# Kernel optimization log

Measured on AMD Instinct MI355X. Metric: run time of the kernel, lower is better.

## Reference

```python
import jax, jax.numpy as jnp
import numpy as np

B, N, G, M = 16, 2048, 128, 32
DM, NL, DI, DS, DTR, DC = 384, 12, 768, 16, 24, 4
EPS = 1e-5


def _silu(x):
    return x * jax.nn.sigmoid(x)


def _ln(x, w, b):
    mu = x.mean(-1, keepdims=True)
    v = ((x - mu) ** 2).mean(-1, keepdims=True)
    return (x - mu) * jax.lax.rsqrt(v + EPS) * w + b


def _bn_eval(x, g, b):
    # eval-mode BatchNorm1d (running mean=0, var=1)
    return x * (g * jax.lax.rsqrt(jnp.float32(1.0) + EPS)) + b


def _fps(pts):
    # farthest point sampling, pts [N,3] -> [G] indices (starts at index 0)
    n = pts.shape[0]
    def body(carry, _):
        dmin, i = carry
        dd = jnp.sum((pts - pts[i]) ** 2, -1)
        dmin = jnp.minimum(dmin, dd)
        return (dmin, jnp.argmax(dmin).astype(jnp.int32)), i
    init = (jnp.full((n,), 1e10, pts.dtype), jnp.array(0, jnp.int32))
    (_, _), idx = jax.lax.scan(body, init, None, length=G)
    return idx


def _group(xyz):
    cidx = jax.vmap(_fps)(xyz)                                   # [B,G]
    center = jnp.take_along_axis(xyz, cidx[..., None], axis=1)    # [B,G,3]
    d2 = jnp.sum((center[:, :, None, :] - xyz[:, None, :, :]) ** 2, -1)  # [B,G,N]
    _, nidx = jax.lax.top_k(-d2, M)                               # [B,G,M]
    nb = jax.vmap(lambda p, i: p[i])(xyz, nidx)                   # [B,G,M,3]
    return nb - center[:, :, None, :], center


def _mixer(x, in_w, cw, cb, xp_w, dt_w, dt_b, A_log, Dp, out_w):
    b, L, _ = x.shape
    xz = jnp.einsum('bld,ed->ble', x, in_w)                       # [B,L,2*DI]
    xin, z = xz[..., :DI], xz[..., DI:]
    xpad = jnp.pad(xin, ((0, 0), (DC - 1, 0), (0, 0)))            # causal depthwise conv
    xin = _silu(sum(xpad[:, k:k + L, :] * cw[:, k] for k in range(DC)) + cb)
    dbl = jnp.einsum('bld,ed->ble', xin, xp_w)                    # [B,L,DTR+2*DS]
    dt = jax.nn.softplus(jnp.einsum('blr,dr->bld', dbl[..., :DTR], dt_w) + dt_b)
    Bm, Cm = dbl[..., DTR:DTR + DS], dbl[..., DTR + DS:]
    A = -jnp.exp(A_log)                                           # [DI,DS]
    dA = jnp.exp(dt[..., None] * A)                               # [B,L,DI,DS]
    dBx = (dt * xin)[..., None] * Bm[:, :, None, :]               # [B,L,DI,DS]
    def step(h, inp):
        dA_t, dBx_t, C_t = inp
        h = dA_t * h + dBx_t
        return h, jnp.einsum('bds,bs->bd', h, C_t)
    h0 = jnp.zeros((b, DI, DS), x.dtype)
    _, ys = jax.lax.scan(step, h0, (jnp.swapaxes(dA, 0, 1), jnp.swapaxes(dBx, 0, 1), jnp.swapaxes(Cm, 0, 1)))
    y = jnp.swapaxes(ys, 0, 1) + Dp * xin
    return jnp.einsum('bld,ed->ble', y * _silu(z), out_w)


def forward_fn(xyz, e1w1, e1b1, bn1g, bn1b, e1w2, e1b2, e2w1, e2b1, bn2g, bn2b,
               e2w2, e2b2, pw1, pb1, pw2, pb2, in_w, conv_w, conv_b, xp_w,
               dt_w, dt_b, A_log, Dp, out_w, lnw, lnb, fnw, fnb):
    nb, center = _group(xyz)
    # Encoder (1x1 convs == pointwise linears) over [B*G, M, 3]
    x = nb.reshape(B * G, M, 3)
    f = jax.nn.relu(_bn_eval(x @ e1w1.T + e1b1, bn1g, bn1b))
    f = f @ e1w2.T + e1b2                                         # [BG,M,256]
    fg = f.max(axis=1, keepdims=True)
    f = jnp.concatenate([jnp.broadcast_to(fg, (B * G, M, 256)), f], -1)
    f = jax.nn.relu(_bn_eval(f @ e2w1.T + e2b1, bn2g, bn2b))
    f = f @ e2w2.T + e2b2                                         # [BG,M,DM]
    tokens = f.max(axis=1).reshape(B, G, DM)
    pos = jax.nn.gelu(center @ pw1.T + pb1) @ pw2.T + pb2
    h = tokens + pos
    residual = None
    for i in range(NL):
        residual = h + residual if residual is not None else h
        h = _mixer(_ln(residual, lnw[i], lnb[i]), in_w[i], conv_w[i], conv_b[i],
                   xp_w[i], dt_w[i], dt_b[i], A_log[i], Dp[i], out_w[i])
    return _ln(h + residual, fnw, fnb)


def setup_inputs() -> dict:
    ks = jax.random.split(jax.random.key(0), 16)
    r = lambda i, s, sc=0.02: jax.random.normal(ks[i], s, jnp.float32) * sc
    dt_init = float(np.log(np.expm1(0.01)))
    return {
        'xyz': jax.random.normal(ks[0], (B, N, 3), jnp.float32),
        'e1w1': r(1, (128, 3), 0.3), 'e1b1': jnp.zeros(128),
        'bn1g': jnp.ones(128), 'bn1b': jnp.zeros(128),
        'e1w2': r(2, (256, 128), 0.05), 'e1b2': jnp.zeros(256),
        'e2w1': r(3, (512, 512), 0.03), 'e2b1': jnp.zeros(512),
        'bn2g': jnp.ones(512), 'bn2b': jnp.zeros(512),
        'e2w2': r(4, (DM, 512), 0.03), 'e2b2': jnp.zeros(DM),
        'pw1': r(5, (128, 3), 0.3), 'pb1': jnp.zeros(128),
        'pw2': r(6, (DM, 128), 0.05), 'pb2': jnp.zeros(DM),
        'in_w': r(7, (NL, 2 * DI, DM)),
        'conv_w': r(8, (NL, DI, DC), 0.2), 'conv_b': jnp.zeros((NL, DI)),
        'xp_w': r(9, (NL, DTR + 2 * DS, DI)),
        'dt_w': r(10, (NL, DI, DTR), 0.1),
        'dt_b': jnp.full((NL, DI), dt_init, jnp.float32),
        'A_log': jnp.log(jnp.broadcast_to(jnp.arange(1, DS + 1, dtype=jnp.float32), (NL, DI, DS)) + 0.0),
        'Dp': jnp.ones((NL, DI)),
        'out_w': r(11, (NL, DM, DI)),
        'lnw': jnp.ones((NL, DM)), 'lnb': jnp.zeros((NL, DM)),
        'fnw': jnp.ones(DM), 'fnb': jnp.zeros(DM),
    }


def reference(xyz, e1w1, e1b1, bn1g, bn1b, e1w2, e1b2, e2w1, e2b1, bn2g, bn2b,
              e2w2, e2b2, pw1, pb1, pw2, pb2, in_w, conv_w, conv_b, xp_w,
              dt_w, dt_b, A_log, Dp, out_w, lnw, lnb, fnw, fnb):
    return forward_fn(xyz, e1w1, e1b1, bn1g, bn1b, e1w2, e1b2, e2w1, e2b1,
                      bn2g, bn2b, e2w2, e2b2, pw1, pb1, pw2, pb2, in_w, conv_w,
                      conv_b, xp_w, dt_w, dt_b, A_log, Dp, out_w, lnw, lnb, fnw, fnb)
```

## Files before the change

### kernel.cpp

```cpp
#include <hip/hip_runtime.h>
#include <hip/hip_bf16.h>
#include <math.h>

#define PN   2048
#define PB   16
#define PG   128
#define PM   32
#define PDM  384
#define PDI  768
#define ROWS 2048

typedef unsigned short ushort_t;
typedef unsigned long long ull_t;
typedef __attribute__((ext_vector_type(8))) short bf8;
typedef __attribute__((ext_vector_type(4))) float f4;

__device__ __forceinline__ ushort_t f2bf(float x) {
  unsigned int u = __float_as_uint(x);
  unsigned int r = (u + 0x7FFFu + ((u >> 16) & 1u)) >> 16;
  return (ushort_t)r;
}
__device__ __forceinline__ ull_t umax64(ull_t a, ull_t b) { return a > b ? a : b; }
__device__ __forceinline__ ull_t umin64(ull_t a, ull_t b) { return a < b ? a : b; }

#define GL2L(gp, lp) __builtin_amdgcn_global_load_lds((const __attribute__((address_space(1))) void*)(gp), (__attribute__((address_space(3))) void*)(lp), 16, 0, 0)

#define CV_O1 32768
#define CV_O2 294912
#define CV_O3 491520
#define CV_O4 7569408
#define CV_TOT 11108352
#define DTWT_TOT (12*768*24)
#define XPWT_TOT (12*192*64*4)
#define PREP_TOT (CV_TOT + DTWT_TOT + XPWT_TOT)
__global__ __launch_bounds__(256) void prep_kernel(
    const float* __restrict__ e1w2, const float* __restrict__ e2w1,
    const float* __restrict__ e2w2, const float* __restrict__ in_w,
    const float* __restrict__ out_w, const float* __restrict__ dt_w,
    const float* __restrict__ xp_w,
    ushort_t* __restrict__ wb, float* __restrict__ dtwT,
    float* __restrict__ xpwT) {
  int i = blockIdx.x*256 + threadIdx.x;
  if (i >= PREP_TOT) return;
  if (i < CV_TOT) {
    const float* s; int off;
    if      (i < CV_O1) { s = e1w2;  off = 0; }
    else if (i < CV_O2) { s = e2w1;  off = CV_O1; }
    else if (i < CV_O3) { s = e2w2;  off = CV_O2; }
    else if (i < CV_O4) { s = in_w;  off = CV_O3; }
    else                { s = out_w; off = CV_O4; }
    wb[i] = f2bf(s[i - off]);
  } else if (i < CV_TOT + DTWT_TOT) {
    int j = i - CV_TOT;
    int layer = j / (768*24);
    int rem = j - layer*768*24;
    int d = rem / 24, r = rem - d*24;
    dtwT[layer*24*768 + r*768 + d] = dt_w[j];
  } else {
    int j = i - CV_TOT - DTWT_TOT;
    int layer = j / 49152;
    int rem = j - layer*49152;
    int r4 = rem >> 8;
    int rem2 = rem & 255;
    int e = rem2 >> 2, jj = rem2 & 3;
    xpwT[j] = (e < 56) ? xp_w[(size_t)layer*56*768 + (size_t)e*768 + r4*4 + jj] : 0.f;
  }
}

__global__ __launch_bounds__(256) void fps_kernel(const float* __restrict__ xyz,
                                                  int* __restrict__ cidx) {
  const int b = blockIdx.x;
  const int tid = threadIdx.x;
  const int wave = tid >> 6, lane = tid & 63;
  __shared__ float pts[PN*3];
  __shared__ ull_t kws[2][4];
  const float* base = xyz + (size_t)b * PN * 3;
  for (int t = tid; t < PN*3; t += 256) pts[t] = base[t];
  __syncthreads();
  float px[8], py[8], pz[8], dmin[8];
  #pragma unroll
  for (int j = 0; j < 8; ++j) {
    int idx = j*256 + tid;
    px[j] = pts[idx*3+0]; py[j] = pts[idx*3+1]; pz[j] = pts[idx*3+2];
    dmin[j] = 1e10f;
  }
  int cur = 0;
  for (int g = 0; g < PG; ++g) {
    if (tid == 0) cidx[b*PG + g] = cur;
    const float cx = pts[cur*3+0], cy = pts[cur*3+1], cz = pts[cur*3+2];
    ull_t k[8];
    #pragma unroll
    for (int j = 0; j < 8; ++j) {
      float dx = __fsub_rn(px[j], cx);
      float dy = __fsub_rn(py[j], cy);
      float dz = __fsub_rn(pz[j], cz);
      float dd = __fadd_rn(__fadd_rn(__fmul_rn(dx,dx), __fmul_rn(dy,dy)), __fmul_rn(dz,dz));
      float dm = fminf(dmin[j], dd);
      dmin[j] = dm;
      k[j] = ((ull_t)__float_as_uint(dm) << 32) | (unsigned)(~(unsigned)(j*256 + tid));
    }
    ull_t a0 = umax64(k[0], k[1]), a1 = umax64(k[2], k[3]);
    ull_t a2 = umax64(k[4], k[5]), a3 = umax64(k[6], k[7]);
    ull_t K = umax64(umax64(a0, a1), umax64(a2, a3));
    #pragma unroll
    for (int off = 1; off < 64; off <<= 1)
      K = umax64(K, (ull_t)__shfl_xor((unsigned long long)K, off));
    const int par = g & 1;
    if (lane == 0) kws[par][wave] = K;
    __syncthreads();
    ull_t K0 = umax64(umax64(kws[par][0], kws[par][1]), umax64(kws[par][2], kws[par][3]));
    cur = (int)(~(unsigned)(K0 & 0xFFFFFFFFull));
  }
}

__global__ __launch_bounds__(64) void knn_kernel(const float* __restrict__ xyz,
                                                 const int* __restrict__ cidx,
                                                 float* __restrict__ nbx,
                                                 float* __restrict__ centerb) {
  const int bg = blockIdx.x;
  const int b = bg >> 7;
  const int lane = threadIdx.x;
  const float* base = xyz + (size_t)b * PN * 3;
  const int ci = cidx[bg];
  const float cx = base[ci*3+0], cy = base[ci*3+1], cz = base[ci*3+2];
  if (lane == 0) { centerb[bg*3+0]=cx; centerb[bg*3+1]=cy; centerb[bg*3+2]=cz; }
  float d2[32];
  #pragma unroll
  for (int j = 0; j < 32; ++j) {
    int idx = j*64 + lane;
    float dx = __fsub_rn(cx, base[idx*3+0]);
    float dy = __fsub_rn(cy, base[idx*3+1]);
    float dz = __fsub_rn(cz, base[idx*3+2]);
    d2[j] = __fadd_rn(__fadd_rn(__fmul_rn(dx,dx), __fmul_rn(dy,dy)), __fmul_rn(dz,dz));
  }
  for (int m = 0; m < PM; ++m) {
    ull_t t[16];
    #pragma unroll
    for (int j = 0; j < 16; ++j) {
      ull_t e0 = ((ull_t)__float_as_uint(d2[j])     << 32) | (unsigned)(j*64 + lane);
      ull_t e1 = ((ull_t)__float_as_uint(d2[j+16])  << 32) | (unsigned)((j+16)*64 + lane);
      t[j] = umin64(e0, e1);
    }
    #pragma unroll
    for (int s = 8; s >= 1; s >>= 1)
      #pragma unroll
      for (int j = 0; j < 16; ++j) if (j < s) t[j] = umin64(t[j], t[j+s]);
    ull_t K = t[0];
    #pragma unroll
    for (int off = 1; off < 64; off <<= 1)
      K = umin64(K, (ull_t)__shfl_xor((unsigned long long)K, off));
    const int k = __builtin_amdgcn_readfirstlane((int)(unsigned)(K & 0xFFFFFFFFull));
    const int jwin = k >> 6, owner = k & 63;
    #pragma unroll
    for (int j = 0; j < 32; ++j)
      if (j == jwin && lane == owner) d2[j] = 1e38f;
    if (lane == 0) {
      nbx[(bg*PM + m)*3 + 0] = base[k*3+0] - cx;
      nbx[(bg*PM + m)*3 + 1] = base[k*3+1] - cy;
      nbx[(bg*PM + m)*3 + 2] = base[k*3+2] - cz;
    }
  }
}

__global__ __launch_bounds__(256) void embed1_kernel(
    const float* __restrict__ nbx,
    const float* __restrict__ e1w1, const float* __restrict__ e1b1,
    const float* __restrict__ bn1g, const float* __restrict__ bn1b,
    const ushort_t* __restrict__ e1w2b, const float* __restrict__ e1b2,
    ushort_t* __restrict__ f2b, ushort_t* __restrict__ fgb) {
  const int bg = blockIdx.x;
  const int tid = threadIdx.x;
  const int wid = tid >> 6, lane = tid & 63;
  const int q = lane >> 4, r16 = lane & 15;
  __shared__ float xs[PM*3];
  __shared__ __align__(16) ushort_t Af[4*2*64*8];
  __shared__ __align__(16) ushort_t Bs[16*64*8];
  if (tid < PM*3) xs[tid] = nbx[bg*PM*3 + tid];
  __syncthreads();
  const float bns = rsqrtf(1.0f + 1e-5f);
  #pragma unroll
  for (int it = 0; it < 16; ++it) {
    int id = tid + it*256;
    int m = id >> 7, c = id & 127;
    float v = xs[m*3+0]*e1w1[c*3+0] + xs[m*3+1]*e1w1[c*3+1] + xs[m*3+2]*e1w1[c*3+2] + e1b1[c];
    v = fmaxf(v * (bn1g[c]*bns) + bn1b[c], 0.0f);
    int kc = c >> 5, cc = c & 31, qq = cc >> 3, j = cc & 7;
    int t = m >> 4, r = m & 15;
    Af[((kc*2 + t)*64 + qq*16 + r)*8 + j] = f2bf(v);
  }
  f4 acc[2][4];
  #pragma unroll
  for (int t = 0; t < 2; ++t)
    #pragma unroll
    for (int jj = 0; jj < 4; ++jj) { f4 z = {0.f,0.f,0.f,0.f}; acc[t][jj] = z; }
  for (int kc = 0; kc < 4; ++kc) {
    #pragma unroll
    for (int u = wid; u < 16; u += 4)
      GL2L(e1w2b + (size_t)(u*16 + r16)*128 + kc*32 + q*8, Bs + u*512);
    __syncthreads();
    bf8 a0 = *(const bf8*)(Af + ((size_t)((kc*2+0)*64 + lane))*8);
    bf8 a1 = *(const bf8*)(Af + ((size_t)((kc*2+1)*64 + lane))*8);
    #pragma unroll
    for (int jj = 0; jj < 4; ++jj) {
      bf8 bv = *(const bf8*)(Bs + ((size_t)((wid*4+jj)*64 + lane))*8);
      acc[0][jj] = __builtin_amdgcn_mfma_f32_16x16x32_bf16(a0, bv, acc[0][jj], 0, 0, 0);
      acc[1][jj] = __builtin_amdgcn_mfma_f32_16x16x32_bf16(a1, bv, acc[1][jj], 0, 0, 0);
    }
    __syncthreads();
  }
  #pragma unroll
  for (int jj = 0; jj < 4; ++jj) {
    const int n = (wid*4+jj)*16 + r16;
    const float bias = e1b2[n];
    float v0[4], v1[4];
    float cm = -1e30f;
    #pragma unroll
    for (int rr = 0; rr < 4; ++rr) {
      v0[rr] = acc[0][jj][rr] + bias;
      v1[rr] = acc[1][jj][rr] + bias;
      cm = fmaxf(cm, fmaxf(v0[rr], v1[rr]));
    }
    cm = fmaxf(cm, __shfl_xor(cm, 16));
    cm = fmaxf(cm, __shfl_xor(cm, 32));
    #pragma unroll
    for (int rr = 0; rr < 4; ++rr) {
      f2b[((size_t)bg*32 + q*4 + rr)*256 + n]      = f2bf(v0[rr]);
      f2b[((size_t)bg*32 + 16 + q*4 + rr)*256 + n] = f2bf(v1[rr]);
    }
    if (lane < 16) fgb[(size_t)bg*256 + n] = f2bf(cm);
  }
}

template<int MT, int NT, int EPI>
__global__ __launch_bounds__(256) void mfma_gemm(
    const ushort_t* __restrict__ A, int lda,
    const ushort_t* __restrict__ W, int ldw,
    float* __restrict__ Cf, ushort_t* __restrict__ Cb, int ldc, int K,
    const float* __restrict__ p0, const float* __restrict__ p1,
    const float* __restrict__ p2, const float* __restrict__ p3) {
  static_assert(EPI != 2 || MT == 4, "groupmax needs MT=4");
  constexpr int AT = 2*MT, BT = 2*NT;
  __shared__ __align__(16) ushort_t As[2*AT*512];
  __shared__ __align__(16) ushort_t Bs[2*BT*512];
  const int tid = threadIdx.x;
  const int wid = tid >> 6, lane = tid & 63;
  const int wr = wid >> 1, wc = wid & 1;
  const int q = lane >> 4, r16 = lane & 15;
  const int m0 = blockIdx.y * (32*MT);
  const int n0 = blockIdx.x * (32*NT);
  f4 acc[MT][NT];
  #pragma unroll
  for (int i = 0; i < MT; ++i)
    #pragma unroll
    for (int j = 0; j < NT; ++j) { f4 z = {0.f,0.f,0.f,0.f}; acc[i][j] = z; }

  for (int k0 = 0; k0 < K; k0 += 64) {
    #pragma unroll
    for (int c = 0; c < 2; ++c) {
      const int kk = k0 + c*32 + q*8;
      #pragma unroll
      for (int t = wid; t < AT; t += 4)
        GL2L(A + (size_t)(m0 + t*16 + r16)*lda + kk, As + (c*AT + t)*512);
      #pragma unroll
      for (int t = wid; t < BT; t += 4)
        GL2L(W + (size_t)(n0 + t*16 + r16)*ldw + kk, Bs + (c*BT + t)*512);
    }
    __syncthreads();
    #pragma unroll
    for (int c = 0; c < 2; ++c) {
      bf8 af[MT], bfr[NT];
      #pragma unroll
      for (int i = 0; i < MT; ++i)
        af[i] = *(const bf8*)(As + ((size_t)(c*AT + wr*MT+i)*64 + lane)*8);
      #pragma unroll
      for (int j = 0; j < NT; ++j)
        bfr[j] = *(const bf8*)(Bs + ((size_t)(c*BT + wc*NT+j)*64 + lane)*8);
      #pragma unroll
      for (int i = 0; i < MT; ++i)
        #pragma unroll
        for (int j = 0; j < NT; ++j)
          acc[i][j] = __builtin_amdgcn_mfma_f32_16x16x32_bf16(af[i], bfr[j], acc[i][j], 0, 0, 0);
    }
    __syncthreads();
  }

  if constexpr (EPI == 0) {
    #pragma unroll
    for (int i = 0; i < MT; ++i) {
      const int row = m0 + (wr*MT+i)*16 + q*4;
      #pragma unroll
      for (int j = 0; j < NT; ++j) {
        const int col = n0 + (wc*NT+j)*16 + r16;
        #pragma unroll
        for (int r = 0; r < 4; ++r)
          Cf[(size_t)(row+r)*ldc + col] = acc[i][j][r];
      }
    }
  } else if constexpr (EPI == 1) {
    const float bns = rsqrtf(1.0f + 1e-5f);
    #pragma unroll
    for (int j = 0; j < NT; ++j) {
      const int col = n0 + (wc*NT+j)*16 + r16;
      const float b1 = p0[col], sg = p1[col]*bns, b2 = p2[col];
      #pragma unroll
      for (int i = 0; i < MT; ++i) {
        const int row = m0 + (wr*MT+i)*16 + q*4;
        #pragma unroll
        for (int r = 0; r < 4; ++r) {
          const int grp = (row + r) >> 5;
          float v = fmaxf(fmaf(acc[i][j][r] + b1 + p3[(size_t)grp*512 + col], sg, b2), 0.0f);
          Cb[(size_t)(row+r)*ldc + col] = f2bf(v);
        }
      }
    }
  } else {
    #pragma unroll
    for (int j = 0; j < NT; ++j) {
      const int col = n0 + (wc*NT+j)*16 + r16;
      float tm[4];
      #pragma unroll
      for (int i = 0; i < 4; ++i) {
        float t = fmaxf(fmaxf(acc[i][j][0], acc[i][j][1]), fmaxf(acc[i][j][2], acc[i][j][3]));
        t = fmaxf(t, __shfl_xor(t, 16));
        t = fmaxf(t, __shfl_xor(t, 32));
        tm[i] = t;
      }
      const float bias = p0[col];
      if (lane < 16) {
        const int g0 = (m0 >> 5) + wr*2;
        Cf[(size_t)g0*ldc + col]     = fmaxf(tm[0], tm[1]) + bias;
        Cf[(size_t)(g0+1)*ldc + col] = fmaxf(tm[2], tm[3]) + bias;
      }
    }
  }
}

__global__ __launch_bounds__(128) void prenorm0_kernel(
    const float* __restrict__ h, const float* __restrict__ centerb,
    const float* __restrict__ pw1, const float* __restrict__ pb1,
    const float* __restrict__ pw2, const float* __restrict__ pb2,
    float* __restrict__ res,
    const float* __restrict__ w, const float* __restrict__ bb,
    ushort_t* __restrict__ xo) {
  const int row = blockIdx.x;
  const int tid = threadIdx.x;
  __shared__ float t1[128];
  __shared__ float s1[2], s2[2];
  const float cx = centerb[row*3+0], cy = centerb[row*3+1], cz = centerb[row*3+2];
  {
    const int c = tid;
    float v = cx*pw1[c*3+0] + cy*pw1[c*3+1] + cz*pw1[c*3+2] + pb1[c];
    float u = 0.7978845608028654f * (v + 0.044715f*v*v*v);
    t1[c] = 0.5f*v*(1.0f + tanhf(u));
  }
  __syncthreads();
  float v[3];
  #pragma unroll
  for (int i = 0; i < 3; ++i) {
    int j = tid + i*128;
    float acc = pb2[j];
    const float4* wp = (const float4*)(pw2 + (size_t)j*128);
    const float4* a = (const float4*)t1;
    for (int k4 = 0; k4 < 32; ++k4) {
      float4 wv = wp[k4], av = a[k4];
      acc = fmaf(av.x, wv.x, fmaf(av.y, wv.y, fmaf(av.z, wv.z, fmaf(av.w, wv.w, acc))));
    }
    float r = h[(size_t)row*PDM + j] + acc;
    res[(size_t)row*PDM + j] = r;
    v[i] = r;
  }
  float ss = v[0] + v[1] + v[2];
  #pragma unroll
  for (int off = 1; off < 64; off <<= 1) ss += __shfl_xor(ss, off);
  if ((tid & 63) == 0) s1[tid>>6] = ss;
  __syncthreads();
  const float mu = (s1[0] + s1[1]) * (1.0f/384.0f);
  float qq = 0.f;
  #pragma unroll
  for (int i = 0; i < 3; ++i) { float d = v[i] - mu; qq += d*d; }
  #pragma unroll
  for (int off = 1; off < 64; off <<= 1) qq += __shfl_xor(qq, off);
  if ((tid & 63) == 0) s2[tid>>6] = qq;
  __syncthreads();
  const float rs = rsqrtf((s2[0] + s2[1]) * (1.0f/384.0f) + 1e-5f);
  #pragma unroll
  for (int i = 0; i < 3; ++i) {
    int j = tid + i*128;
    xo[(size_t)row*PDM + j] = f2bf((v[i] - mu) * rs * w[j] + bb[j]);
  }
}

__global__ __launch_bounds__(128) void prenorm_kernel(
    const float* __restrict__ h, float* __restrict__ res,
    const float* __restrict__ w, const float* __restrict__ bb,
    ushort_t* __restrict__ xo) {
  const int row = blockIdx.x;
  const int tid = threadIdx.x;
  __shared__ float s1[2], s2[2];
  float v[3];
  #pragma unroll
  for (int i = 0; i < 3; ++i) {
    int j = tid + i*128;
    float r = h[(size_t)row*PDM + j] + res[(size_t)row*PDM + j];
    res[(size_t)row*PDM + j] = r;
    v[i] = r;
  }
  float ss = v[0] + v[1] + v[2];
  #pragma unroll
  for (int off = 1; off < 64; off <<= 1) ss += __shfl_xor(ss, off);
  if ((tid & 63) == 0) s1[tid>>6] = ss;
  __syncthreads();
  const float mu = (s1[0] + s1[1]) * (1.0f/384.0f);
  float qq = 0.f;
  #pragma unroll
  for (int i = 0; i < 3; ++i) { float d = v[i] - mu; qq += d*d; }
  #pragma unroll
  for (int off = 1; off < 64; off <<= 1) qq += __shfl_xor(qq, off);
  if ((tid & 63) == 0) s2[tid>>6] = qq;
  __syncthreads();
  const float rs = rsqrtf((s2[0] + s2[1]) * (1.0f/384.0f) + 1e-5f);
  #pragma unroll
  for (int i = 0; i < 3; ++i) {
    int j = tid + i*128;
    xo[(size_t)row*PDM + j] = f2bf((v[i] - mu) * rs * w[j] + bb[j]);
  }
}

__global__ __launch_bounds__(128) void final_kernel(
    const float* __restrict__ h, const float* __restrict__ res,
    const float* __restrict__ w, const float* __restrict__ bb,
    float* __restrict__ out) {
  const int row = blockIdx.x;
  const int tid = threadIdx.x;
  __shared__ float s1[2], s2[2];
  float v[3];
  #pragma unroll
  for (int i = 0; i < 3; ++i) {
    int j = tid + i*128;
    v[i] = h[(size_t)row*PDM + j] + res[(size_t)row*PDM + j];
  }
  float ss = v[0] + v[1] + v[2];
  #pragma unroll
  for (int off = 1; off < 64; off <<= 1) ss += __shfl_xor(ss, off);
  if ((tid & 63) == 0) s1[tid>>6] = ss;
  __syncthreads();
  const float mu = (s1[0] + s1[1]) * (1.0f/384.0f);
  float qq = 0.f;
  #pragma unroll
  for (int i = 0; i < 3; ++i) { float d = v[i] - mu; qq += d*d; }
  #pragma unroll
  for (int off = 1; off < 64; off <<= 1) qq += __shfl_xor(qq, off);
  if ((tid & 63) == 0) s2[tid>>6] = qq;
  __syncthreads();
  const float rs = rsqrtf((s2[0] + s2[1]) * (1.0f/384.0f) + 1e-5f);
  #pragma unroll
  for (int i = 0; i < 3; ++i) {
    int j = tid + i*128;
    out[(size_t)row*PDM + j] = (v[i] - mu) * rs * w[j] + bb[j];
  }
}

__global__ __launch_bounds__(256) void cxd_kernel(
    const float* __restrict__ xz,
    const float* __restrict__ cw, const float* __restrict__ cb,
    const float* __restrict__ xpwT,
    const float* __restrict__ dtwT, const float* __restrict__ dtbias,
    float* __restrict__ xin, float* __restrict__ dbl, float* __restrict__ dtg) {
  const int row = blockIdx.x;
  const int tid = threadIdx.x;
  const int wid = tid >> 6, lane = tid & 63;
  const int l = row & 127;
  const int bb = row - l;
  __shared__ float xin_s[PDI];
  __shared__ float part[4][64];
  __shared__ float dbl_s[64];
  #pragma unroll
  for (int i = 0; i < 3; ++i) {
    const int d = tid + i*256;
    float acc = cb[d];
    #pragma unroll
    for (int k = 0; k < 4; ++k) {
      int ll = l + k - 3;
      if (ll >= 0) acc = fmaf(xz[(size_t)(bb+ll)*1536 + d], cw[d*4+k], acc);
    }
    float s = 1.0f / (1.0f + __expf(-acc));
    float v = acc * s;
    xin_s[d] = v;
    xin[(size_t)row*PDI + d] = v;
  }
  __syncthreads();
  {
    const float4* wp = (const float4*)xpwT;
    float a = 0.f;
    const int base_r4 = wid*48;
    for (int t = 0; t < 48; ++t) {
      const int r4 = base_r4 + t;
      float4 w4 = wp[r4*64 + lane];
      float4 x4 = *(const float4*)&xin_s[r4*4];
      a = fmaf(x4.x, w4.x, fmaf(x4.y, w4.y, fmaf(x4.z, w4.z, fmaf(x4.w, w4.w, a))));
    }
    part[wid][lane] = a;
  }
  __syncthreads();
  if (tid < 64) {
    float v = part[0][tid] + part[1][tid] + part[2][tid] + part[3][tid];
    dbl_s[tid] = v;
    if (tid < 56) dbl[(size_t)row*56 + tid] = v;
  }
  __syncthreads();
  #pragma unroll
  for (int i = 0; i < 3; ++i) {
    const int d = tid + i*256;
    float acc = dtbias[d];
    #pragma unroll
    for (int r = 0; r < 24; ++r) acc = fmaf(dbl_s[r], dtwT[r*768 + d], acc);
    dtg[(size_t)row*PDI + d] = log1pf(expf(-fabsf(acc))) + fmaxf(acc, 0.0f);
  }
}

__global__ __launch_bounds__(256) void scan_kernel(const float* __restrict__ dt,
                                                   const float* __restrict__ xin,
                                                   const float* __restrict__ dbl,
                                                   const float* __restrict__ alog,
                                                   const float* __restrict__ dp,
                                                   const float* __restrict__ xz,
                                                   ushort_t* __restrict__ yb) {
  const int s = threadIdx.x & 15;
  const int dl = threadIdx.x >> 4;
  const int d = blockIdx.x*16 + dl;
  const int b = blockIdx.y;
  const float A = -expf(alog[d*16 + s]);
  const float Dv = dp[d];
  float h = 0.f;
  int ro = b*128;
  float dtv = dt[(size_t)ro*PDI + d];
  float xv  = xin[(size_t)ro*PDI + d];
  float Bv  = dbl[(size_t)ro*56 + 24 + s];
  float Cv  = dbl[(size_t)ro*56 + 40 + s];
  float zv  = xz[(size_t)ro*1536 + 768 + d];
  for (int l = 0; l < 128; ++l) {
    float ndt = 0.f, nxv = 0.f, nBv = 0.f, nCv = 0.f, nz = 0.f;
    const int r2 = ro + 1;
    if (l < 127) {
      ndt = dt[(size_t)r2*PDI + d];
      nxv = xin[(size_t)r2*PDI + d];
      nBv = dbl[(size_t)r2*56 + 24 + s];
      nCv = dbl[(size_t)r2*56 + 40 + s];
      nz  = xz[(size_t)r2*1536 + 768 + d];
    }
    float dA = __expf(dtv * A);
    h = fmaf(dA, h, dtv * xv * Bv);
    float p = h * Cv;
    p += __shfl_xor(p, 1);
    p += __shfl_xor(p, 2);
    p += __shfl_xor(p, 4);
    p += __shfl_xor(p, 8);
    if (s == 0) {
      float sg = 1.0f / (1.0f + __expf(-zv));
      yb[(size_t)ro*PDI + d] = f2bf(fmaf(Dv, xv, p) * zv * sg);
    }
    dtv = ndt; xv = nxv; Bv = nBv; Cv = nCv; zv = nz;
    ro = r2;
  }
}

extern "C" void kernel_launch(void* const* d_in, const int* in_sizes, int n_in,
                              void* d_out, int out_size, void* d_ws, size_t ws_size,
                              hipStream_t stream) {
  const float* xyz    = (const float*)d_in[0];
  const float* e1w1   = (const float*)d_in[1];
  const float* e1b1   = (const float*)d_in[2];
  const float* bn1g   = (const float*)d_in[3];
  const float* bn1b   = (const float*)d_in[4];
  const float* e1w2   = (const float*)d_in[5];
  const float* e1b2   = (const float*)d_in[6];
  const float* e2w1   = (const float*)d_in[7];
  const float* e2b1   = (const float*)d_in[8];
  const float* bn2g   = (const float*)d_in[9];
  const float* bn2b   = (const float*)d_in[10];
  const float* e2w2   = (const float*)d_in[11];
  const float* e2b2   = (const float*)d_in[12];
  const float* pw1    = (const float*)d_in[13];
  const float* pb1    = (const float*)d_in[14];
  const float* pw2    = (const float*)d_in[15];
  const float* pb2    = (const float*)d_in[16];
  const float* in_w   = (const float*)d_in[17];
  const float* conv_w = (const float*)d_in[18];
  const float* conv_b = (const float*)d_in[19];
  const float* xp_w   = (const float*)d_in[20];
  const float* dt_w   = (const float*)d_in[21];
  const float* dt_b   = (const float*)d_in[22];
  const float* A_log  = (const float*)d_in[23];
  const float* Dp     = (const float*)d_in[24];
  const float* out_w  = (const float*)d_in[25];
  const float* lnw    = (const float*)d_in[26];
  const float* lnb    = (const float*)d_in[27];
  const float* fnw    = (const float*)d_in[28];
  const float* fnb    = (const float*)d_in[29];

  char* ws = (char*)d_ws;
  size_t off = 0;
  auto alloc = [&](size_t bytes) { void* p = ws + off; off += (bytes + 255) & ~(size_t)255; return p; };
  int*      cidx    = (int*)     alloc(PB*PG*4);
  float*    centerb = (float*)   alloc(ROWS*3*4);
  float*    nbx     = (float*)   alloc(ROWS*PM*3*4);
  ushort_t* f2b     = (ushort_t*)alloc((size_t)ROWS*PM*256*2);
  ushort_t* fgb     = (ushort_t*)alloc((size_t)ROWS*256*2);
  float*    gbuf    = (float*)   alloc((size_t)ROWS*512*4);
  ushort_t* f3      = (ushort_t*)alloc((size_t)ROWS*PM*512*2);
  float*    hbuf    = (float*)   alloc((size_t)ROWS*PDM*4);
  float*    resid   = (float*)   alloc((size_t)ROWS*PDM*4);
  ushort_t* xlnb    = (ushort_t*)alloc((size_t)ROWS*PDM*2);
  float*    xz      = (float*)   alloc((size_t)ROWS*1536*4);
  float*    xin     = (float*)   alloc((size_t)ROWS*PDI*4);
  float*    dbl     = (float*)   alloc((size_t)ROWS*56*4);
  float*    dtg     = (float*)   alloc((size_t)ROWS*PDI*4);
  ushort_t* ybufb   = (ushort_t*)alloc((size_t)ROWS*PDI*2);
  ushort_t* wb      = (ushort_t*)alloc((size_t)CV_TOT*2);
  float*    dtwT    = (float*)   alloc((size_t)DTWT_TOT*4);
  float*    xpwT    = (float*)   alloc((size_t)XPWT_TOT*4);

  ushort_t* e1w2b  = wb;
  ushort_t* e2w1b  = wb + CV_O1;
  ushort_t* e2w2b  = wb + CV_O2;
  ushort_t* in_wb  = wb + CV_O3;
  ushort_t* out_wb = wb + CV_O4;

  prep_kernel<<<(PREP_TOT+255)/256, 256, 0, stream>>>(
      e1w2, e2w1, e2w2, in_w, out_w, dt_w, xp_w, wb, dtwT, xpwT);

  fps_kernel<<<PB, 256, 0, stream>>>(xyz, cidx);
  knn_kernel<<<ROWS, 64, 0, stream>>>(xyz, cidx, nbx, centerb);
  embed1_kernel<<<ROWS, 256, 0, stream>>>(nbx, e1w1, e1b1, bn1g, bn1b, e1w2b, e1b2, f2b, fgb);

  mfma_gemm<2,4,0><<<dim3(4, 32), 256, 0, stream>>>(
      fgb, 256, e2w1b, 512, gbuf, nullptr, 512, 256, nullptr, nullptr, nullptr, nullptr);
  mfma_gemm<4,4,1><<<dim3(4, 512), 256, 0, stream>>>(
      f2b, 256, e2w1b + 256, 512, nullptr, f3, 512, 256, e2b1, bn2g, bn2b, gbuf);
  mfma_gemm<4,4,2><<<dim3(3, 512), 256, 0, stream>>>(
      f3, 512, e2w2b, 512, hbuf, nullptr, PDM, 512, e2b2, nullptr, nullptr, nullptr);

  prenorm0_kernel<<<ROWS, 128, 0, stream>>>(hbuf, centerb, pw1, pb1, pw2, pb2,
                                            resid, lnw, lnb, xlnb);

  for (int i = 0; i < 12; ++i) {
    mfma_gemm<2,4,0><<<dim3(12, 32), 256, 0, stream>>>(
        xlnb, PDM, in_wb + (size_t)i*1536*384, PDM, xz, nullptr, 1536, PDM,
        nullptr, nullptr, nullptr, nullptr);
    cxd_kernel<<<ROWS, 256, 0, stream>>>(
        xz, conv_w + (size_t)i*768*4, conv_b + (size_t)i*768,
        xpwT + (size_t)i*49152, dtwT + (size_t)i*24*768, dt_b + (size_t)i*768,
        xin, dbl, dtg);
    scan_kernel<<<dim3(48, PB), 256, 0, stream>>>(
        dtg, xin, dbl, A_log + (size_t)i*768*16, Dp + (size_t)i*768, xz, ybufb);
    mfma_gemm<2,2,0><<<dim3(6, 32), 256, 0, stream>>>(
        ybufb, PDI, out_wb + (size_t)i*384*768, PDI, hbuf, nullptr, PDM, PDI,
        nullptr, nullptr, nullptr, nullptr);
    if (i < 11)
      prenorm_kernel<<<ROWS, 128, 0, stream>>>(hbuf, resid, lnw + (i+1)*384, lnb + (i+1)*384, xlnb);
    else
      final_kernel<<<ROWS, 128, 0, stream>>>(hbuf, resid, fnw, fnb, (float*)d_out);
  }
}
```

Before: 1.841 ms.

## Store xz/xin in bf16, fuse dt projection into scan, stage scan inputs in LDS

The in_proj GEMM gets a new epilogue that writes xz as bf16, and the conv kernel writes xin as bf16, halving intermediate traffic. The dt projection and softplus move from cxd_kernel into scan_kernel, which removes the dtg buffer round trip. The scan now stages dbl, xin, z and dt in shared memory, reduces over the 16 state lanes with DPP instead of shuffles, and writes y through LDS in coalesced stores. The bf16 intermediates cost some precision, and the dt projection is now computed per scan block.

```diff
diff --git a/kernel.cpp b/kernel.cpp
--- a/kernel.cpp
+++ b/kernel.cpp
@@ -11,6 +11,7 @@
 #define ROWS 2048
 
 typedef unsigned short ushort_t;
+typedef unsigned int uint_t;
 typedef unsigned long long ull_t;
 typedef __attribute__((ext_vector_type(8))) short bf8;
 typedef __attribute__((ext_vector_type(4))) float f4;
@@ -20,8 +21,19 @@
   unsigned int r = (u + 0x7FFFu + ((u >> 16) & 1u)) >> 16;
   return (ushort_t)r;
 }
+__device__ __forceinline__ float bf2f(ushort_t u) {
+  return __uint_as_float(((unsigned)u) << 16);
+}
 __device__ __forceinline__ ull_t umax64(ull_t a, ull_t b) { return a > b ? a : b; }
 __device__ __forceinline__ ull_t umin64(ull_t a, ull_t b) { return a < b ? a : b; }
+
+__device__ __forceinline__ float rowsum16(float v) {
+  v += __int_as_float(__builtin_amdgcn_update_dpp(0, __float_as_int(v), 0x121, 0xF, 0xF, false));
+  v += __int_as_float(__builtin_amdgcn_update_dpp(0, __float_as_int(v), 0x122, 0xF, 0xF, false));
+  v += __int_as_float(__builtin_amdgcn_update_dpp(0, __float_as_int(v), 0x124, 0xF, 0xF, false));
+  v += __int_as_float(__builtin_amdgcn_update_dpp(0, __float_as_int(v), 0x128, 0xF, 0xF, false));
+  return v;
+}
 
 #define GL2L(gp, lp) __builtin_amdgcn_global_load_lds((const __attribute__((address_space(1))) void*)(gp), (__attribute__((address_space(3))) void*)(lp), 16, 0, 0)
 
@@ -313,6 +325,18 @@
         }
       }
     }
+  } else if constexpr (EPI == 3) {
+    #pragma unroll
+    for (int i = 0; i < MT; ++i) {
+      const int row = m0 + (wr*MT+i)*16 + q*4;
+      #pragma unroll
+      for (int j = 0; j < NT; ++j) {
+        const int col = n0 + (wc*NT+j)*16 + r16;
+        #pragma unroll
+        for (int r = 0; r < 4; ++r)
+          Cb[(size_t)(row+r)*ldc + col] = f2bf(acc[i][j][r]);
+      }
+    }
   } else {
     #pragma unroll
     for (int j = 0; j < NT; ++j) {
@@ -461,11 +485,10 @@
 }
 
 __global__ __launch_bounds__(256) void cxd_kernel(
-    const float* __restrict__ xz,
+    const ushort_t* __restrict__ xzb,
     const float* __restrict__ cw, const float* __restrict__ cb,
     const float* __restrict__ xpwT,
-    const float* __restrict__ dtwT, const float* __restrict__ dtbias,
-    float* __restrict__ xin, float* __restrict__ dbl, float* __restrict__ dtg) {
+    ushort_t* __restrict__ xinb, float* __restrict__ dbl) {
   const int row = blockIdx.x;
   const int tid = threadIdx.x;
   const int wid = tid >> 6, lane = tid & 63;
@@ -473,7 +496,6 @@
   const int bb = row - l;
   __shared__ float xin_s[PDI];
   __shared__ float part[4][64];
-  __shared__ float dbl_s[64];
   #pragma unroll
   for (int i = 0; i < 3; ++i) {
     const int d = tid + i*256;
@@ -481,12 +503,12 @@
     #pragma unroll
     for (int k = 0; k < 4; ++k) {
       int ll = l + k - 3;
-      if (ll >= 0) acc = fmaf(xz[(size_t)(bb+ll)*1536 + d], cw[d*4+k], acc);
+      if (ll >= 0) acc = fmaf(bf2f(xzb[(size_t)(bb+ll)*1536 + d]), cw[d*4+k], acc);
     }
     float s = 1.0f / (1.0f + __expf(-acc));
     float v = acc * s;
     xin_s[d] = v;
-    xin[(size_t)row*PDI + d] = v;
+    xinb[(size_t)row*PDI + d] = f2bf(v);
   }
   __syncthreads();
   {
@@ -504,63 +526,73 @@
   __syncthreads();
   if (tid < 64) {
     float v = part[0][tid] + part[1][tid] + part[2][tid] + part[3][tid];
-    dbl_s[tid] = v;
     if (tid < 56) dbl[(size_t)row*56 + tid] = v;
   }
-  __syncthreads();
-  #pragma unroll
-  for (int i = 0; i < 3; ++i) {
-    const int d = tid + i*256;
-    float acc = dtbias[d];
-    #pragma unroll
-    for (int r = 0; r < 24; ++r) acc = fmaf(dbl_s[r], dtwT[r*768 + d], acc);
-    dtg[(size_t)row*PDI + d] = log1pf(expf(-fabsf(acc))) + fmaxf(acc, 0.0f);
-  }
-}
-
-__global__ __launch_bounds__(256) void scan_kernel(const float* __restrict__ dt,
-                                                   const float* __restrict__ xin,
-                                                   const float* __restrict__ dbl,
-                                                   const float* __restrict__ alog,
-                                                   const float* __restrict__ dp,
-                                                   const float* __restrict__ xz,
-                                                   ushort_t* __restrict__ yb) {
-  const int s = threadIdx.x & 15;
-  const int dl = threadIdx.x >> 4;
-  const int d = blockIdx.x*16 + dl;
-  const int b = blockIdx.y;
+}
+
+__global__ __launch_bounds__(256) void scan_kernel(
+    const ushort_t* __restrict__ xzb,
+    const ushort_t* __restrict__ xinb,
+    const float* __restrict__ dbl,
+    const float* __restrict__ dtwT, const float* __restrict__ dtbias,
+    const float* __restrict__ alog, const float* __restrict__ dp,
+    ushort_t* __restrict__ yb) {
+  const int d0 = blockIdx.x * 16;
+  const int b  = blockIdx.y;
+  const int tid = threadIdx.x;
+  __shared__ float dbl_s[128*56];
+  __shared__ float dts[128*16];
+  __shared__ float dtw_s[24*16];
+  __shared__ ushort_t xins[128*16];
+  __shared__ ushort_t zs[128*16];
+  __shared__ ushort_t ys[128*16];
+  {
+    const float4* src = (const float4*)(dbl + (size_t)b*128*56);
+    float4* dst = (float4*)dbl_s;
+    for (int i = tid; i < 1792; i += 256) dst[i] = src[i];
+  }
+  for (int i = tid; i < 24*16; i += 256) {
+    int r = i >> 4, c = i & 15;
+    dtw_s[i] = dtwT[r*768 + d0 + c];
+  }
+  for (int i = tid; i < 1024; i += 256) {
+    int l = i >> 3, c2 = (i & 7)*2;
+    *(uint_t*)&xins[l*16 + c2] = *(const uint_t*)(xinb + ((size_t)(b*128 + l))*768 + d0 + c2);
+    *(uint_t*)&zs[l*16 + c2]   = *(const uint_t*)(xzb + ((size_t)(b*128 + l))*1536 + 768 + d0 + c2);
+  }
+  __syncthreads();
+  for (int i = tid; i < 2048; i += 256) {
+    int l = i >> 4, c = i & 15;
+    float acc = dtbias[d0 + c];
+    #pragma unroll
+    for (int r = 0; r < 24; ++r) acc = fmaf(dbl_s[l*56 + r], dtw_s[r*16 + c], acc);
+    dts[i] = log1pf(expf(-fabsf(acc))) + fmaxf(acc, 0.0f);
+  }
+  __syncthreads();
+  const int s = tid & 15, dl = tid >> 4;
+  const int d = d0 + dl;
   const float A = -expf(alog[d*16 + s]);
   const float Dv = dp[d];
   float h = 0.f;
-  int ro = b*128;
-  float dtv = dt[(size_t)ro*PDI + d];
-  float xv  = xin[(size_t)ro*PDI + d];
-  float Bv  = dbl[(size_t)ro*56 + 24 + s];
-  float Cv  = dbl[(size_t)ro*56 + 40 + s];
-  float zv  = xz[(size_t)ro*1536 + 768 + d];
+  #pragma unroll 4
   for (int l = 0; l < 128; ++l) {
-    float ndt = 0.f, nxv = 0.f, nBv = 0.f, nCv = 0.f, nz = 0.f;
-    const int r2 = ro + 1;
-    if (l < 127) {
-      ndt = dt[(size_t)r2*PDI + d];
-      nxv = xin[(size_t)r2*PDI + d];
-      nBv = dbl[(size_t)r2*56 + 24 + s];
-      nCv = dbl[(size_t)r2*56 + 40 + s];
-      nz  = xz[(size_t)r2*1536 + 768 + d];
-    }
+    float dtv = dts[l*16 + dl];
+    float xv  = bf2f(xins[l*16 + dl]);
+    float Bv  = dbl_s[l*56 + 24 + s];
+    float Cv  = dbl_s[l*56 + 40 + s];
     float dA = __expf(dtv * A);
     h = fmaf(dA, h, dtv * xv * Bv);
-    float p = h * Cv;
-    p += __shfl_xor(p, 1);
-    p += __shfl_xor(p, 2);
-    p += __shfl_xor(p, 4);
-    p += __shfl_xor(p, 8);
+    float p = rowsum16(h * Cv);
     if (s == 0) {
-      float sg = 1.0f / (1.0f + __expf(-zv));
-      yb[(size_t)ro*PDI + d] = f2bf(fmaf(Dv, xv, p) * zv * sg);
-    }
-    dtv = ndt; xv = nxv; Bv = nBv; Cv = nCv; zv = nz;
-    ro = r2;
+      float z = bf2f(zs[l*16 + dl]);
+      float sg = 1.0f / (1.0f + __expf(-z));
+      ys[l*16 + dl] = f2bf(fmaf(Dv, xv, p) * z * sg);
+    }
+  }
+  __syncthreads();
+  for (int i = tid; i < 1024; i += 256) {
+    int l = i >> 3, c2 = (i & 7)*2;
+    *(uint_t*)(yb + ((size_t)(b*128 + l))*768 + d0 + c2) = *(const uint_t*)&ys[l*16 + c2];
   }
 }
 
@@ -611,10 +643,9 @@
   float*    hbuf    = (float*)   alloc((size_t)ROWS*PDM*4);
   float*    resid   = (float*)   alloc((size_t)ROWS*PDM*4);
   ushort_t* xlnb    = (ushort_t*)alloc((size_t)ROWS*PDM*2);
-  float*    xz      = (float*)   alloc((size_t)ROWS*1536*4);
-  float*    xin     = (float*)   alloc((size_t)ROWS*PDI*4);
+  ushort_t* xzb     = (ushort_t*)alloc((size_t)ROWS*1536*2);
+  ushort_t* xinb    = (ushort_t*)alloc((size_t)ROWS*PDI*2);
   float*    dbl     = (float*)   alloc((size_t)ROWS*56*4);
-  float*    dtg     = (float*)   alloc((size_t)ROWS*PDI*4);
   ushort_t* ybufb   = (ushort_t*)alloc((size_t)ROWS*PDI*2);
   ushort_t* wb      = (ushort_t*)alloc((size_t)CV_TOT*2);
   float*    dtwT    = (float*)   alloc((size_t)DTWT_TOT*4);
@@ -644,15 +675,15 @@
                                             resid, lnw, lnb, xlnb);
 
   for (int i = 0; i < 12; ++i) {
-    mfma_gemm<2,4,0><<<dim3(12, 32), 256, 0, stream>>>(
-        xlnb, PDM, in_wb + (size_t)i*1536*384, PDM, xz, nullptr, 1536, PDM,
+    mfma_gemm<2,4,3><<<dim3(12, 32), 256, 0, stream>>>(
+        xlnb, PDM, in_wb + (size_t)i*1536*384, PDM, nullptr, xzb, 1536, PDM,
         nullptr, nullptr, nullptr, nullptr);
     cxd_kernel<<<ROWS, 256, 0, stream>>>(
-        xz, conv_w + (size_t)i*768*4, conv_b + (size_t)i*768,
-        xpwT + (size_t)i*49152, dtwT + (size_t)i*24*768, dt_b + (size_t)i*768,
-        xin, dbl, dtg);
+        xzb, conv_w + (size_t)i*768*4, conv_b + (size_t)i*768,
+        xpwT + (size_t)i*49152, xinb, dbl);
     scan_kernel<<<dim3(48, PB), 256, 0, stream>>>(
-        dtg, xin, dbl, A_log + (size_t)i*768*16, Dp + (size_t)i*768, xz, ybufb);
+        xzb, xinb, dbl, dtwT + (size_t)i*24*768, dt_b + (size_t)i*768,
+        A_log + (size_t)i*768*16, Dp + (size_t)i*768, ybufb);
     mfma_gemm<2,2,0><<<dim3(6, 32), 256, 0, stream>>>(
         ybufb, PDI, out_wb + (size_t)i*384*768, PDI, hbuf, nullptr, PDM, PDI,
         nullptr, nullptr, nullptr, nullptr);
```

New measurement: 1.543 ms. -16.2%, faster.
